# Performance work log

Measured on AMD Instinct MI355X. Metric: run time of the kernel, lower is better.

The kernel has to match this reference:

```python
import jax, jax.numpy as jnp
from jax import lax
import numpy as np

VOCAB = 100
EMBED = 16
STATE = 7
OUT = 10
B, T = 4096, 512


def setup_inputs() -> dict:
    key = jax.random.key(0)
    k0, k1, k2, k3, k4 = jax.random.split(key, 5)
    tokens = jax.random.randint(k0, (B, T), 0, VOCAB, dtype=jnp.int32)
    emb = jax.random.normal(k1, (VOCAB, EMBED), dtype=jnp.float32) * 0.05
    # LSTMCell params, Keras gate order: i, f, g(candidate), o
    W = jax.random.normal(k2, (EMBED, 4 * STATE), dtype=jnp.float32) * 0.1
    U = jax.random.normal(k3, (STATE, 4 * STATE), dtype=jnp.float32) * 0.1
    # unit_forget_bias=True in Keras: forget-gate bias initialized to 1
    b = jnp.concatenate([jnp.zeros(STATE), jnp.ones(STATE), jnp.zeros(2 * STATE)]).astype(jnp.float32)
    Wd = jax.random.normal(k4, (STATE, OUT), dtype=jnp.float32) * 0.1
    bd = jnp.zeros((OUT,), dtype=jnp.float32)
    return {"tokens": tokens, "emb": emb, "W": W, "U": U, "b": b, "Wd": Wd, "bd": bd}


def reference(tokens, emb, W, U, b, Wd, bd):
    x = emb[tokens]                      # [B, T, E] embedding lookup
    x_tm = jnp.swapaxes(x, 0, 1)         # [T, B, E] time-major for scan

    def step(carry, xt):
        h, c = carry                     # [B, S] each
        z = xt @ W + h @ U + b           # [B, 4S]
        zi, zf, zg, zo = jnp.split(z, 4, axis=-1)
        i = jax.nn.sigmoid(zi)
        f = jax.nn.sigmoid(zf)
        g = jnp.tanh(zg)
        o = jax.nn.sigmoid(zo)
        c_new = f * c + i * g
        h_new = o * jnp.tanh(c_new)
        return (h_new, c_new), h_new

    h0 = jnp.zeros((tokens.shape[0], STATE), dtype=x.dtype)
    c0 = jnp.zeros_like(h0)
    _, hs = lax.scan(step, (h0, c0), x_tm)   # hs: [T, B, S]
    h_seq = jnp.swapaxes(hs, 0, 1)           # [B, T, S]
    logits = h_seq @ Wd + bd                 # [B, T, 10]
    return jax.nn.softmax(logits, axis=-1)
```

## Files before the change

kernel.cpp:

```cpp
#include <hip/hip_runtime.h>

#define VOCABN 100
#define EMBEDN 16
#define STATEN 7
#define OUTN   10
#define BATCHN 4096
#define SEQT   512
#define L2E 1.44269504088896340736f

typedef float v2f __attribute__((ext_vector_type(2)));

__device__ __forceinline__ float fexp2(float x){ float r; asm("v_exp_f32 %0, %1":"=v"(r):"v"(x)); return r; }
__device__ __forceinline__ float frcp (float x){ float r; asm("v_rcp_f32 %0, %1":"=v"(r):"v"(x)); return r; }

template<int C> __device__ __forceinline__ int dppi(int x){
  return __builtin_amdgcn_update_dpp(0, x, C, 0xF, 0xF, true);
}
template<int C> __device__ __forceinline__ float dppf(float x){
  return __int_as_float(__builtin_amdgcn_update_dpp(0, __float_as_int(x), C, 0xF, 0xF, true));
}

__global__ void embw_kernel(const float* __restrict__ emb, const float* __restrict__ W,
                            const float* __restrict__ b, float* __restrict__ embw){
  int v = blockIdx.x, j = threadIdx.x;
  int pos = j >> 1, g2 = j & 1;
  int s = pos >> 1, p = pos & 1, gate = p*2 + g2;
  float val = 0.0f;
  if (s < STATEN) {
    int col = gate*STATEN + s;
    val = b[col];
    #pragma unroll
    for (int e = 0; e < EMBEDN; ++e) val = fmaf(emb[v*EMBEDN+e], W[e*28+col], val);
    val *= (gate == 2) ? (2.0f*L2E) : (-L2E);
  }
  embw[v*32 + pos*2 + g2] = val;
}

__global__ void __launch_bounds__(64,1)
lstm_kernel(const int* __restrict__ tokens, const float* __restrict__ embw,
            const float* __restrict__ U, const float* __restrict__ Wd,
            const float* __restrict__ bdv, float* __restrict__ out){
  __shared__ float embW_s[VOCABN*32];
  __shared__ int   tok_s[4*520];
  __shared__ float hbuf[2*8*48 + 64];

  const int L = threadIdx.x;
  const int b0 = blockIdx.x*4;

  for (int i=L;i<VOCABN*8;i+=64) ((float4*)embW_s)[i]=((const float4*)embw)[i];
  for (int i=L;i<512;i+=64){ int r=i>>7,c4=i&127;
    int4 v=((const int4*)(tokens+(size_t)(b0+r)*SEQT))[c4];
    *((int4*)&tok_s[r*520+c4*4])=v; }
  if (L<4){ tok_s[L*520+512]=0; tok_s[L*520+513]=0; tok_s[L*520+514]=0; }
  __syncthreads();

  const int pos=L&15, ch=L>>4, s=pos>>1, p=pos&1;
  const int pos2=pos*2;

  int sg[8];
  sg[0]=s;
  sg[1]=dppi<0x122>(s); sg[2]=dppi<0x124>(s); sg[3]=dppi<0x126>(s);
  sg[4]=dppi<0x128>(s); sg[5]=dppi<0x12A>(s); sg[6]=dppi<0x12C>(s); sg[7]=dppi<0x12E>(s);

  v2f Ucp[8];
  {
    const int gA=p*2, gB=p*2+1;
    const float sA = (gA==2)?(2.0f*L2E):(-L2E);
    const float sB = (gB==2)?(2.0f*L2E):(-L2E);
    #pragma unroll
    for (int k=0;k<8;++k){
      int sk=sg[k]; bool vld=(sk<STATEN)&&(s<STATEN);
      Ucp[k].x = vld ? U[sk*28+gA*7+s]*sA : 0.0f;
      Ucp[k].y = vld ? U[sk*28+gB*7+s]*sB : 0.0f;
    }
  }
  float Wdc[8][5], bdr[5];
  #pragma unroll
  for (int k=0;k<8;++k)
    #pragma unroll
    for (int o=0;o<5;++o) Wdc[k][o] = (k<STATEN)? Wd[k*10+p*5+o]*L2E : 0.0f;
  #pragma unroll
  for (int o=0;o<5;++o) bdr[o]=bdv[p*5+o]*L2E;

  const int* trow=&tok_s[ch*520];
  float* outp = out + ((size_t)(b0+ch)*SEQT + s)*OUTN + p*5;

  const int loff = p ? (2*8*48 + L) : (ch*8 + s);
  const int roff = s*48 + ch*8;

  float hc[8], lg[5], ee[5];
  float smq=0.0f, rs=0.0f;

  int tok_next = trow[1];
  v2f pf0 = *(const v2f*)&embW_s[trow[0]*32 + pos2];
  float Cc=0.0f, h=0.0f;

  for (int m=0;m<64;++m){
    const int* trm = trow + m*8;
    float* wv = hbuf + (m&1)*384 + loff;
    const float* rv = hbuf + ((m+1)&1)*384 + roff;
    #pragma unroll
    for (int u=0;u<8;++u){
      int tokN = trm[u+2];
      v2f pfN = *(const v2f*)&embW_s[tok_next*32 + pos2];

      float r0=h;
      float r1=dppf<0x122>(h), r2=dppf<0x124>(h), r3=dppf<0x126>(h);
      float r4=dppf<0x128>(h), r5=dppf<0x12A>(h), r6=dppf<0x12C>(h), r7=dppf<0x12E>(h);

      v2f z01=__builtin_elementwise_fma((v2f){r1,r1},Ucp[1],
              __builtin_elementwise_fma((v2f){r0,r0},Ucp[0],pf0));
      v2f z23=__builtin_elementwise_fma((v2f){r3,r3},Ucp[3],(v2f){r2,r2}*Ucp[2]);
      v2f z45=__builtin_elementwise_fma((v2f){r5,r5},Ucp[5],(v2f){r4,r4}*Ucp[4]);
      v2f z67=__builtin_elementwise_fma((v2f){r7,r7},Ucp[7],(v2f){r6,r6}*Ucp[6]);
      v2f zv=(z01+z23)+(z45+z67);

      float gA=frcp(1.0f+fexp2(zv.x));
      float gB=frcp(1.0f+fexp2(zv.y));
      float gg_s=__builtin_fmaf(gA,-4.0f*L2E,2.0f*L2E);
      float gg_x=dppf<0xB1>(gg_s);
      float go_x=dppf<0xB1>(gB);
      Cc=__builtin_fmaf(gB,Cc,gA*gg_x);
      float rcpC=frcp(1.0f+fexp2(Cc));
      float rcpC_x=dppf<0xB1>(rcpC);
      float go_u = p ? gB     : go_x;
      float rc_u = p ? rcpC_x : rcpC;
      h=__builtin_fmaf(-2.0f*go_u, rc_u, go_u);

      wv[u*48] = h;

      if (u==0){
        float4 a = *(const float4*)rv;
        float4 bq = *(const float4*)(rv+4);
        hc[0]=a.x; hc[1]=a.y; hc[2]=a.z; hc[3]=a.w;
        hc[4]=bq.x; hc[5]=bq.y; hc[6]=bq.z; hc[7]=bq.w;
      }
      if (u==1){
        float a0=bdr[0], a1=bdr[1];
        #pragma unroll
        for (int k=0;k<8;++k){ a0=__builtin_fmaf(hc[k],Wdc[k][0],a0);
                               a1=__builtin_fmaf(hc[k],Wdc[k][1],a1); }
        lg[0]=a0; lg[1]=a1; }
      if (u==2){
        float a2=bdr[2], a3=bdr[3];
        #pragma unroll
        for (int k=0;k<8;++k){ a2=__builtin_fmaf(hc[k],Wdc[k][2],a2);
                               a3=__builtin_fmaf(hc[k],Wdc[k][3],a3); }
        lg[2]=a2; lg[3]=a3; }
      if (u==3){
        float a4=bdr[4];
        #pragma unroll
        for (int k=0;k<8;++k) a4=__builtin_fmaf(hc[k],Wdc[k][4],a4);
        lg[4]=a4; }
      if (u==4){
        ee[0]=fexp2(lg[0]); ee[1]=fexp2(lg[1]); ee[2]=fexp2(lg[2]);
        ee[3]=fexp2(lg[3]); ee[4]=fexp2(lg[4]); }
      if (u==5){
        smq=((ee[0]+ee[1])+(ee[2]+ee[3]))+ee[4]; }
      if (u==6){
        rs=frcp(smq + dppf<0xB1>(smq)); }
      if (u==7){
        if (m>=1){
          outp[0]=ee[0]*rs; outp[1]=ee[1]*rs; outp[2]=ee[2]*rs;
          outp[3]=ee[3]*rs; outp[4]=ee[4]*rs;
          outp += 8*OUTN;
        } }

      pf0=pfN; tok_next=tokN;
    }
  }

  {
    const float* rv = hbuf + 384 + roff;
    float4 a = *(const float4*)rv;
    float4 bq = *(const float4*)(rv+4);
    hc[0]=a.x; hc[1]=a.y; hc[2]=a.z; hc[3]=a.w;
    hc[4]=bq.x; hc[5]=bq.y; hc[6]=bq.z; hc[7]=bq.w;
    #pragma unroll
    for (int o=0;o<5;++o){ float aa=bdr[o];
      #pragma unroll
      for (int k=0;k<8;++k) aa=__builtin_fmaf(hc[k],Wdc[k][o],aa);
      lg[o]=aa; }
    float e0=fexp2(lg[0]), e1=fexp2(lg[1]), e2=fexp2(lg[2]),
          e3=fexp2(lg[3]), e4=fexp2(lg[4]);
    float sm=((e0+e1)+(e2+e3))+e4;
    float r=frcp(sm + dppf<0xB1>(sm));
    outp[0]=e0*r; outp[1]=e1*r; outp[2]=e2*r; outp[3]=e3*r; outp[4]=e4*r;
  }
}

extern "C" void kernel_launch(void* const* d_in, const int* in_sizes, int n_in,
                              void* d_out, int out_size, void* d_ws, size_t ws_size,
                              hipStream_t stream) {
  const int*   tokens = (const int*)d_in[0];
  const float* emb    = (const float*)d_in[1];
  const float* W      = (const float*)d_in[2];
  const float* U      = (const float*)d_in[3];
  const float* b      = (const float*)d_in[4];
  const float* Wd     = (const float*)d_in[5];
  const float* bd     = (const float*)d_in[6];
  float* outp = (float*)d_out;
  float* embw = (float*)d_ws;

  embw_kernel<<<dim3(VOCABN), dim3(32), 0, stream>>>(emb, W, b, embw);
  lstm_kernel<<<dim3(BATCHN/4), dim3(64), 0, stream>>>(tokens, embw, U, Wd, bd, outp);
}
```

Baseline: 78.96 us.

## Compute all four gates per lane and pack eight sequences per wave

Each lane now evaluates all four LSTM gates for one state unit instead of splitting gate pairs across two lanes. This removes the cross-lane DPP exchanges on the recurrence's critical path and lets one 64-lane wave carry eight batch rows instead of four, halving the block count. The embedding-projection table is written in a rotated layout so each lane reads its four gate values with one float4 load without bank conflicts. The output projection and softmax now cover all ten outputs per lane, trading more per-lane arithmetic and registers for fewer waves and shorter dependency chains.

```diff
diff --git a/kernel.cpp b/kernel.cpp
--- a/kernel.cpp
+++ b/kernel.cpp
@@ -23,8 +23,7 @@
 __global__ void embw_kernel(const float* __restrict__ emb, const float* __restrict__ W,
                             const float* __restrict__ b, float* __restrict__ embw){
   int v = blockIdx.x, j = threadIdx.x;
-  int pos = j >> 1, g2 = j & 1;
-  int s = pos >> 1, p = pos & 1, gate = p*2 + g2;
+  int s = j >> 2, gate = j & 3;
   float val = 0.0f;
   if (s < STATEN) {
     int col = gate*STATEN + s;
@@ -33,7 +32,7 @@
     for (int e = 0; e < EMBEDN; ++e) val = fmaf(emb[v*EMBEDN+e], W[e*28+col], val);
     val *= (gate == 2) ? (2.0f*L2E) : (-L2E);
   }
-  embw[v*32 + pos*2 + g2] = val;
+  embw[v*32 + ((s+v)&7)*4 + gate] = val;
 }
 
 __global__ void __launch_bounds__(64,1)
@@ -41,93 +40,96 @@
             const float* __restrict__ U, const float* __restrict__ Wd,
             const float* __restrict__ bdv, float* __restrict__ out){
   __shared__ float embW_s[VOCABN*32];
-  __shared__ int   tok_s[4*520];
-  __shared__ float hbuf[2*8*48 + 64];
+  __shared__ int   tok_s[8*520];
+  __shared__ float hring[2*8*64];
 
   const int L = threadIdx.x;
-  const int b0 = blockIdx.x*4;
+  const int b0 = blockIdx.x*8;
 
   for (int i=L;i<VOCABN*8;i+=64) ((float4*)embW_s)[i]=((const float4*)embw)[i];
-  for (int i=L;i<512;i+=64){ int r=i>>7,c4=i&127;
+  for (int i=L;i<8*128;i+=64){ int r=i>>7,c4=i&127;
     int4 v=((const int4*)(tokens+(size_t)(b0+r)*SEQT))[c4];
     *((int4*)&tok_s[r*520+c4*4])=v; }
-  if (L<4){ tok_s[L*520+512]=0; tok_s[L*520+513]=0; tok_s[L*520+514]=0; }
+  if (L<8){ tok_s[L*520+512]=0; tok_s[L*520+513]=0; tok_s[L*520+514]=0; }
   __syncthreads();
 
-  const int pos=L&15, ch=L>>4, s=pos>>1, p=pos&1;
-  const int pos2=pos*2;
+  const int pos=L&15, row=L>>4, s=pos>>1, q=pos&1;
+  const int ch = row*2 + q;
 
   int sg[8];
   sg[0]=s;
   sg[1]=dppi<0x122>(s); sg[2]=dppi<0x124>(s); sg[3]=dppi<0x126>(s);
   sg[4]=dppi<0x128>(s); sg[5]=dppi<0x12A>(s); sg[6]=dppi<0x12C>(s); sg[7]=dppi<0x12E>(s);
 
-  v2f Ucp[8];
-  {
-    const int gA=p*2, gB=p*2+1;
-    const float sA = (gA==2)?(2.0f*L2E):(-L2E);
-    const float sB = (gB==2)?(2.0f*L2E):(-L2E);
-    #pragma unroll
-    for (int k=0;k<8;++k){
-      int sk=sg[k]; bool vld=(sk<STATEN)&&(s<STATEN);
-      Ucp[k].x = vld ? U[sk*28+gA*7+s]*sA : 0.0f;
-      Ucp[k].y = vld ? U[sk*28+gB*7+s]*sB : 0.0f;
-    }
-  }
-  float Wdc[8][5], bdr[5];
+  v2f Uif[8], Ugo[8];
   #pragma unroll
-  for (int k=0;k<8;++k)
-    #pragma unroll
-    for (int o=0;o<5;++o) Wdc[k][o] = (k<STATEN)? Wd[k*10+p*5+o]*L2E : 0.0f;
+  for (int k=0;k<8;++k){
+    int sk=sg[k]; bool vld=(sk<STATEN)&&(s<STATEN);
+    Uif[k].x = vld ? U[sk*28 + 0*7 + s]*(-L2E)     : 0.0f;
+    Uif[k].y = vld ? U[sk*28 + 1*7 + s]*(-L2E)     : 0.0f;
+    Ugo[k].x = vld ? U[sk*28 + 2*7 + s]*(2.0f*L2E) : 0.0f;
+    Ugo[k].y = vld ? U[sk*28 + 3*7 + s]*(-L2E)     : 0.0f;
+  }
+
+  const int chf = L>>3, tq = L&7;
+  float Wdf[7][10], bdf[10];
   #pragma unroll
-  for (int o=0;o<5;++o) bdr[o]=bdv[p*5+o]*L2E;
+  for (int k=0;k<7;++k)
+    #pragma unroll
+    for (int o=0;o<OUTN;++o) Wdf[k][o] = Wd[k*10+o]*L2E;
+  #pragma unroll
+  for (int o=0;o<OUTN;++o) bdf[o]=bdv[o]*L2E;
 
   const int* trow=&tok_s[ch*520];
-  float* outp = out + ((size_t)(b0+ch)*SEQT + s)*OUTN + p*5;
-
-  const int loff = p ? (2*8*48 + L) : (ch*8 + s);
-  const int roff = s*48 + ch*8;
-
-  float hc[8], lg[5], ee[5];
-  float smq=0.0f, rs=0.0f;
+  float* outp = out + ((size_t)(b0+chf)*SEQT + tq)*OUTN;
+
+  const int hoff = ch*8 + s;
+  const int roff = tq*64 + chf*8;
+
+  float hc[8], lg[10], ee[10];
+  float rs=0.0f;
 
   int tok_next = trow[1];
-  v2f pf0 = *(const v2f*)&embW_s[trow[0]*32 + pos2];
+  float4 pf0 = *(const float4*)&embW_s[trow[0]*32 + (((s+trow[0])&7)<<2)];
   float Cc=0.0f, h=0.0f;
 
   for (int m=0;m<64;++m){
     const int* trm = trow + m*8;
-    float* wv = hbuf + (m&1)*384 + loff;
-    const float* rv = hbuf + ((m+1)&1)*384 + roff;
+    float* wv = hring + (m&1)*512;
+    const float* rv = hring + ((m+1)&1)*512 + roff;
     #pragma unroll
     for (int u=0;u<8;++u){
       int tokN = trm[u+2];
-      v2f pfN = *(const v2f*)&embW_s[tok_next*32 + pos2];
+      float4 pfN = *(const float4*)&embW_s[tok_next*32 + (((s+tok_next)&7)<<2)];
 
       float r0=h;
       float r1=dppf<0x122>(h), r2=dppf<0x124>(h), r3=dppf<0x126>(h);
       float r4=dppf<0x128>(h), r5=dppf<0x12A>(h), r6=dppf<0x12C>(h), r7=dppf<0x12E>(h);
 
-      v2f z01=__builtin_elementwise_fma((v2f){r1,r1},Ucp[1],
-              __builtin_elementwise_fma((v2f){r0,r0},Ucp[0],pf0));
-      v2f z23=__builtin_elementwise_fma((v2f){r3,r3},Ucp[3],(v2f){r2,r2}*Ucp[2]);
-      v2f z45=__builtin_elementwise_fma((v2f){r5,r5},Ucp[5],(v2f){r4,r4}*Ucp[4]);
-      v2f z67=__builtin_elementwise_fma((v2f){r7,r7},Ucp[7],(v2f){r6,r6}*Ucp[6]);
-      v2f zv=(z01+z23)+(z45+z67);
-
-      float gA=frcp(1.0f+fexp2(zv.x));
-      float gB=frcp(1.0f+fexp2(zv.y));
-      float gg_s=__builtin_fmaf(gA,-4.0f*L2E,2.0f*L2E);
-      float gg_x=dppf<0xB1>(gg_s);
-      float go_x=dppf<0xB1>(gB);
-      Cc=__builtin_fmaf(gB,Cc,gA*gg_x);
-      float rcpC=frcp(1.0f+fexp2(Cc));
-      float rcpC_x=dppf<0xB1>(rcpC);
-      float go_u = p ? gB     : go_x;
-      float rc_u = p ? rcpC_x : rcpC;
-      h=__builtin_fmaf(-2.0f*go_u, rc_u, go_u);
-
-      wv[u*48] = h;
+      v2f zif = {pf0.x, pf0.y}, zgo = {pf0.z, pf0.w};
+      v2f a01 = __builtin_elementwise_fma((v2f){r1,r1},Uif[1],
+                __builtin_elementwise_fma((v2f){r0,r0},Uif[0],zif));
+      v2f a23 = __builtin_elementwise_fma((v2f){r3,r3},Uif[3],(v2f){r2,r2}*Uif[2]);
+      v2f a45 = __builtin_elementwise_fma((v2f){r5,r5},Uif[5],(v2f){r4,r4}*Uif[4]);
+      v2f a67 = __builtin_elementwise_fma((v2f){r7,r7},Uif[7],(v2f){r6,r6}*Uif[6]);
+      zif = (a01+a23)+(a45+a67);
+      v2f b01 = __builtin_elementwise_fma((v2f){r1,r1},Ugo[1],
+                __builtin_elementwise_fma((v2f){r0,r0},Ugo[0],zgo));
+      v2f b23 = __builtin_elementwise_fma((v2f){r3,r3},Ugo[3],(v2f){r2,r2}*Ugo[2]);
+      v2f b45 = __builtin_elementwise_fma((v2f){r5,r5},Ugo[5],(v2f){r4,r4}*Ugo[4]);
+      v2f b67 = __builtin_elementwise_fma((v2f){r7,r7},Ugo[7],(v2f){r6,r6}*Ugo[6]);
+      zgo = (b01+b23)+(b45+b67);
+
+      float gi = frcp(1.0f+fexp2(zif.x));
+      float gf = frcp(1.0f+fexp2(zif.y));
+      float rg = frcp(1.0f+fexp2(zgo.x));
+      float go = frcp(1.0f+fexp2(zgo.y));
+      float gg_s = __builtin_fmaf(rg,-4.0f*L2E,2.0f*L2E);
+      Cc = __builtin_fmaf(gf, Cc, gi*gg_s);
+      float rcpC = frcp(1.0f+fexp2(Cc));
+      h = __builtin_fmaf(-2.0f*go, rcpC, go);
+
+      wv[u*64 + hoff] = h;
 
       if (u==0){
         float4 a = *(const float4*)rv;
@@ -136,33 +138,41 @@
         hc[4]=bq.x; hc[5]=bq.y; hc[6]=bq.z; hc[7]=bq.w;
       }
       if (u==1){
-        float a0=bdr[0], a1=bdr[1];
         #pragma unroll
-        for (int k=0;k<8;++k){ a0=__builtin_fmaf(hc[k],Wdc[k][0],a0);
-                               a1=__builtin_fmaf(hc[k],Wdc[k][1],a1); }
-        lg[0]=a0; lg[1]=a1; }
+        for (int o=0;o<4;++o){ float a=bdf[o];
+          #pragma unroll
+          for (int k=0;k<7;++k) a=__builtin_fmaf(hc[k],Wdf[k][o],a);
+          lg[o]=a; } }
       if (u==2){
-        float a2=bdr[2], a3=bdr[3];
         #pragma unroll
-        for (int k=0;k<8;++k){ a2=__builtin_fmaf(hc[k],Wdc[k][2],a2);
-                               a3=__builtin_fmaf(hc[k],Wdc[k][3],a3); }
-        lg[2]=a2; lg[3]=a3; }
+        for (int o=4;o<8;++o){ float a=bdf[o];
+          #pragma unroll
+          for (int k=0;k<7;++k) a=__builtin_fmaf(hc[k],Wdf[k][o],a);
+          lg[o]=a; } }
       if (u==3){
-        float a4=bdr[4];
         #pragma unroll
-        for (int k=0;k<8;++k) a4=__builtin_fmaf(hc[k],Wdc[k][4],a4);
-        lg[4]=a4; }
+        for (int o=8;o<OUTN;++o){ float a=bdf[o];
+          #pragma unroll
+          for (int k=0;k<7;++k) a=__builtin_fmaf(hc[k],Wdf[k][o],a);
+          lg[o]=a; } }
       if (u==4){
         ee[0]=fexp2(lg[0]); ee[1]=fexp2(lg[1]); ee[2]=fexp2(lg[2]);
         ee[3]=fexp2(lg[3]); ee[4]=fexp2(lg[4]); }
       if (u==5){
-        smq=((ee[0]+ee[1])+(ee[2]+ee[3]))+ee[4]; }
+        ee[5]=fexp2(lg[5]); ee[6]=fexp2(lg[6]); ee[7]=fexp2(lg[7]);
+        ee[8]=fexp2(lg[8]); ee[9]=fexp2(lg[9]); }
       if (u==6){
-        rs=frcp(smq + dppf<0xB1>(smq)); }
+        float sm=(((ee[0]+ee[1])+(ee[2]+ee[3]))+((ee[4]+ee[5])+(ee[6]+ee[7])))
+                 +(ee[8]+ee[9]);
+        rs=frcp(sm); }
       if (u==7){
         if (m>=1){
-          outp[0]=ee[0]*rs; outp[1]=ee[1]*rs; outp[2]=ee[2]*rs;
-          outp[3]=ee[3]*rs; outp[4]=ee[4]*rs;
+          float2* op=(float2*)outp;
+          op[0]=make_float2(ee[0]*rs,ee[1]*rs);
+          op[1]=make_float2(ee[2]*rs,ee[3]*rs);
+          op[2]=make_float2(ee[4]*rs,ee[5]*rs);
+          op[3]=make_float2(ee[6]*rs,ee[7]*rs);
+          op[4]=make_float2(ee[8]*rs,ee[9]*rs);
           outp += 8*OUTN;
         } }
 
@@ -171,21 +181,27 @@
   }
 
   {
-    const float* rv = hbuf + 384 + roff;
+    const float* rv = hring + 512 + roff;
     float4 a = *(const float4*)rv;
     float4 bq = *(const float4*)(rv+4);
     hc[0]=a.x; hc[1]=a.y; hc[2]=a.z; hc[3]=a.w;
-    hc[4]=bq.x; hc[5]=bq.y; hc[6]=bq.z; hc[7]=bq.w;
-    #pragma unroll
-    for (int o=0;o<5;++o){ float aa=bdr[o];
+    hc[4]=bq.x; hc[5]=bq.y; hc[6]=bq.z;
+    #pragma unroll
+    for (int o=0;o<OUTN;++o){ float aa=bdf[o];
       #pragma unroll
-      for (int k=0;k<8;++k) aa=__builtin_fmaf(hc[k],Wdc[k][o],aa);
+      for (int k=0;k<7;++k) aa=__builtin_fmaf(hc[k],Wdf[k][o],aa);
       lg[o]=aa; }
-    float e0=fexp2(lg[0]), e1=fexp2(lg[1]), e2=fexp2(lg[2]),
-          e3=fexp2(lg[3]), e4=fexp2(lg[4]);
-    float sm=((e0+e1)+(e2+e3))+e4;
-    float r=frcp(sm + dppf<0xB1>(sm));
-    outp[0]=e0*r; outp[1]=e1*r; outp[2]=e2*r; outp[3]=e3*r; outp[4]=e4*r;
+    float e0=fexp2(lg[0]), e1=fexp2(lg[1]), e2=fexp2(lg[2]), e3=fexp2(lg[3]),
+          e4=fexp2(lg[4]), e5=fexp2(lg[5]), e6=fexp2(lg[6]), e7=fexp2(lg[7]),
+          e8=fexp2(lg[8]), e9=fexp2(lg[9]);
+    float sm=(((e0+e1)+(e2+e3))+((e4+e5)+(e6+e7)))+(e8+e9);
+    float r=frcp(sm);
+    float2* op=(float2*)outp;
+    op[0]=make_float2(e0*r,e1*r);
+    op[1]=make_float2(e2*r,e3*r);
+    op[2]=make_float2(e4*r,e5*r);
+    op[3]=make_float2(e6*r,e7*r);
+    op[4]=make_float2(e8*r,e9*r);
   }
 }
 
@@ -203,5 +219,5 @@
   float* embw = (float*)d_ws;
 
   embw_kernel<<<dim3(VOCABN), dim3(32), 0, stream>>>(emb, W, b, embw);
-  lstm_kernel<<<dim3(BATCHN/4), dim3(64), 0, stream>>>(tokens, embw, U, Wd, bd, outp);
-}
+  lstm_kernel<<<dim3(BATCHN/8), dim3(64), 0, stream>>>(tokens, embw, U, Wd, bd, outp);
+}
```

Result: slower. 108.1 us (+36.9%).
